# Kernel tuning notes

Hardware: AMD Instinct MI355X
Metric: run time of the kernel (lower is better)

Reference implementation:

```python
import jax, jax.numpy as jnp
import numpy as np

EPS = 1e-08
ORDINAL = 2.0

def setup_inputs() -> dict:
    key = jax.random.key(0)
    k1, k2, k3, k4, k5 = jax.random.split(key, 5)
    B, IN, OUT = 1024, 256, 1024
    inputs = jax.random.normal(k1, (B, IN), dtype=jnp.float32)
    weights = jax.random.normal(k2, (OUT, IN), dtype=jnp.float32) * (1.0 / np.sqrt(IN))
    biases = jax.random.normal(k3, (OUT,), dtype=jnp.float32) * (1.0 / np.sqrt(IN))
    centers = jax.random.normal(k4, (OUT, IN), dtype=jnp.float32) * 0.1
    # diag inv covars ~ U(3/(IN+0.5), 3/(IN-0.5)) per reset_parameters
    inv_covars = jax.random.uniform(k5, (OUT, IN), dtype=jnp.float32,
                                    minval=3.0 / (IN + 0.5), maxval=3.0 / (IN - 0.5))
    return {"inputs": inputs, "weights": weights, "biases": biases,
            "centers": centers, "inv_covars": inv_covars}

def reference(inputs, weights, biases, centers, inv_covars):
    # linear part: [B, OUT]
    l = inputs @ weights.T + biases
    # diag covar path (ordinal = 2.0, so the 1e-32 stabilizer is absent and
    # pow(c^2, 1/ordinal) == |c| after clamping):
    # g[b, z] = sum_i ( |x[b,i] - c[z,i]| * sqrt(clamp(ic[z,i])^2) )^2
    ic = jnp.minimum(inv_covars, 1.0 / EPS)
    scale = jnp.power(ic * ic, 1.0 / ORDINAL)  # [OUT, IN]
    diff = jnp.abs(inputs[:, None, :] - centers[None, :, :]) * scale[None, :, :]  # [B, OUT, IN]
    g = jnp.exp(-jnp.sum(jnp.power(diff, ORDINAL), axis=-1))  # [B, OUT]
    res = l * g
    return (res, g)
```

## Files before the change

### kernel.cpp

```cpp
#include <hip/hip_runtime.h>
#include <hip/hip_bf16.h>
#include <math.h>


typedef __attribute__((ext_vector_type(8))) short short8;
typedef __attribute__((ext_vector_type(4))) float floatx4;

#define MFMA __builtin_amdgcn_mfma_f32_16x16x32_bf16
#define INDIM 256
#define OUTD  1024
#define BD    1024
#define TM 64
#define TN 32
#define TK 64
#define KSTR 72

__device__ __forceinline__ unsigned pkbf(float a, float b) {
    union { __hip_bfloat162 h; unsigned u; } v;
    v.h = __float22bfloat162_rn(make_float2(a, b));
    return v.u;
}

__global__ __launch_bounds__(256)
void fgn_fused(const float* __restrict__ X, const float* __restrict__ W,
               const float* __restrict__ Bias, const float* __restrict__ C,
               const float* __restrict__ IC, float* __restrict__ Out)
{
    __shared__ __align__(16) unsigned short As [TM * KSTR];
    __shared__ __align__(16) unsigned short As2[TM * KSTR];
    __shared__ __align__(16) unsigned short Bw [TN * KSTR];
    __shared__ __align__(16) unsigned short Bg1[TN * KSTR];
    __shared__ __align__(16) unsigned short Bg2[TN * KSTR];
    __shared__ __align__(16) unsigned short Bg3[TN * KSTR];

    const int b    = blockIdx.x;
    const int xcd  = b & 7;
    const int i    = b >> 3;
    const int ncol = xcd + 8 * (i & 3);
    const int mrow = i >> 2;
    const int n0   = ncol * TN;
    const int m0   = mrow * TM;

    const int t    = threadIdx.x;
    const int w    = t >> 6;
    const int lane = t & 63;
    const int r    = lane & 15;
    const int q    = lane >> 4;

    const int arow = t >> 2;
    const int akq  = (t & 3) << 4;
    const int bz   = t >> 3;
    const int bkq  = (t & 7) << 3;

    floatx4 zero = {0.f, 0.f, 0.f, 0.f};
    floatx4 accL[2] = {zero, zero};
    floatx4 accG[2] = {zero, zero};
    floatx4 accC[2] = {zero, zero};
    short8 ones;
    #pragma unroll
    for (int iq = 0; iq < 8; ++iq) ones[iq] = (short)0x3F80;

    for (int k0 = 0; k0 < INDIM; k0 += TK) {
        float4 xa[4];
        {
            const float* xp = &X[(size_t)(m0 + arow) * INDIM + k0 + akq];
            #pragma unroll
            for (int j = 0; j < 4; ++j) xa[j] = ((const float4*)xp)[j];
        }
        const size_t bo = (size_t)(n0 + bz) * INDIM + k0 + bkq;
        float4 wv0 = *(const float4*)&W[bo],  wv1 = *(const float4*)&W[bo + 4];
        float4 cv0 = *(const float4*)&C[bo],  cv1 = *(const float4*)&C[bo + 4];
        float4 iv0 = *(const float4*)&IC[bo], iv1 = *(const float4*)&IC[bo + 4];

        __syncthreads();

        {
            const float* xf = (const float*)xa;
            unsigned ux[8], ux2[8];
            #pragma unroll
            for (int j = 0; j < 8; ++j) {
                float e0 = xf[2*j], e1 = xf[2*j+1];
                ux[j]  = pkbf(e0, e1);
                ux2[j] = pkbf(e0 * e0, e1 * e1);
            }
            uint4* pa  = (uint4*)&As [arow * KSTR + akq];
            uint4* pa2 = (uint4*)&As2[arow * KSTR + akq];
            pa[0]  = make_uint4(ux[0],  ux[1],  ux[2],  ux[3]);
            pa[1]  = make_uint4(ux[4],  ux[5],  ux[6],  ux[7]);
            pa2[0] = make_uint4(ux2[0], ux2[1], ux2[2], ux2[3]);
            pa2[1] = make_uint4(ux2[4], ux2[5], ux2[6], ux2[7]);
        }
        {
            float wf[8] = {wv0.x,wv0.y,wv0.z,wv0.w, wv1.x,wv1.y,wv1.z,wv1.w};
            float cf[8] = {cv0.x,cv0.y,cv0.z,cv0.w, cv1.x,cv1.y,cv1.z,cv1.w};
            float f0[8] = {iv0.x,iv0.y,iv0.z,iv0.w, iv1.x,iv1.y,iv1.z,iv1.w};
            float g1[8], g2[8], g3[8];
            #pragma unroll
            for (int j = 0; j < 8; ++j) {
                float s  = fminf(f0[j], 1e8f);
                float qq = s * s;
                g2[j] = qq;
                g1[j] = -2.f * cf[j] * qq;
                g3[j] = cf[j] * cf[j] * qq;
            }
            const int bb = bz * KSTR + bkq;
            *(uint4*)&Bw [bb] = make_uint4(pkbf(wf[0],wf[1]), pkbf(wf[2],wf[3]),
                                           pkbf(wf[4],wf[5]), pkbf(wf[6],wf[7]));
            *(uint4*)&Bg1[bb] = make_uint4(pkbf(g1[0],g1[1]), pkbf(g1[2],g1[3]),
                                           pkbf(g1[4],g1[5]), pkbf(g1[6],g1[7]));
            *(uint4*)&Bg2[bb] = make_uint4(pkbf(g2[0],g2[1]), pkbf(g2[2],g2[3]),
                                           pkbf(g2[4],g2[5]), pkbf(g2[6],g2[7]));
            *(uint4*)&Bg3[bb] = make_uint4(pkbf(g3[0],g3[1]), pkbf(g3[2],g3[3]),
                                           pkbf(g3[4],g3[5]), pkbf(g3[6],g3[7]));
        }
        __syncthreads();

        #pragma unroll
        for (int kk = 0; kk < 2; ++kk) {
            const int ko = kk * 32 + q * 8;
            short8 a0 = *(const short8*)&As [(w * 16 + r) * KSTR + ko];
            short8 a2 = *(const short8*)&As2[(w * 16 + r) * KSTR + ko];
            #pragma unroll
            for (int nt = 0; nt < 2; ++nt) {
                const int br = (nt * 16 + r) * KSTR + ko;
                short8 bwf = *(const short8*)&Bw [br];
                short8 b1f = *(const short8*)&Bg1[br];
                short8 b2f = *(const short8*)&Bg2[br];
                short8 b3f = *(const short8*)&Bg3[br];
                accL[nt] = MFMA(a0,   bwf, accL[nt], 0, 0, 0);
                accG[nt] = MFMA(a0,   b1f, accG[nt], 0, 0, 0);
                accG[nt] = MFMA(a2,   b2f, accG[nt], 0, 0, 0);
                accC[nt] = MFMA(ones, b3f, accC[nt], 0, 0, 0);
            }
        }
    }

    float* OutR = Out;
    float* OutG = Out + (size_t)BD * OUTD;
    #pragma unroll
    for (int nt = 0; nt < 2; ++nt) {
        const int n     = n0 + nt * 16 + r;
        const float bias = Bias[n];
        const float cz   = accC[nt][0];
        #pragma unroll
        for (int reg = 0; reg < 4; ++reg) {
            const int m = m0 + w * 16 + q * 4 + reg;
            const float g   = expf(-(accG[nt][reg] + cz));
            const float res = (accL[nt][reg] + bias) * g;
            OutR[(size_t)m * OUTD + n] = res;
            OutG[(size_t)m * OUTD + n] = g;
        }
    }
}

extern "C" void kernel_launch(void* const* d_in, const int* in_sizes, int n_in,
                              void* d_out, int out_size, void* d_ws, size_t ws_size,
                              hipStream_t stream) {
    const float* X    = (const float*)d_in[0];
    const float* W    = (const float*)d_in[1];
    const float* Bias = (const float*)d_in[2];
    const float* C    = (const float*)d_in[3];
    const float* IC   = (const float*)d_in[4];
    float* Out = (float*)d_out;

    fgn_fused<<<512, 256, 0, stream>>>(X, W, Bias, C, IC, Out);
}
```

Baseline: 71.55 us.

## Double K-tile size, prefetch next tile, compute center-norm term in fp32

Raises the K tile from 64 to 128, so the kernel runs two iterations, and software-pipelines them by issuing the second tile's global loads before computing on the first. The per-output constant sum c^2*ic^2 is no longer a fourth MFMA against a ones vector. Each thread accumulates it in fp32 and a shuffle reduction writes it to shared memory, which drops one MFMA chain and one LDS buffer. The cost is higher register pressure from the larger prefetch buffers, with launch bounds now requesting two blocks per CU.

```diff
diff --git a/kernel.cpp b/kernel.cpp
--- a/kernel.cpp
+++ b/kernel.cpp
@@ -12,8 +12,8 @@
 #define BD    1024
 #define TM 64
 #define TN 32
-#define TK 64
-#define KSTR 72
+#define TK 128
+#define KSTR 136
 
 __device__ __forceinline__ unsigned pkbf(float a, float b) {
     union { __hip_bfloat162 h; unsigned u; } v;
@@ -21,7 +21,7 @@
     return v.u;
 }
 
-__global__ __launch_bounds__(256)
+__global__ __launch_bounds__(256, 2)
 void fgn_fused(const float* __restrict__ X, const float* __restrict__ W,
                const float* __restrict__ Bias, const float* __restrict__ C,
                const float* __restrict__ IC, float* __restrict__ Out)
@@ -31,15 +31,13 @@
     __shared__ __align__(16) unsigned short Bw [TN * KSTR];
     __shared__ __align__(16) unsigned short Bg1[TN * KSTR];
     __shared__ __align__(16) unsigned short Bg2[TN * KSTR];
-    __shared__ __align__(16) unsigned short Bg3[TN * KSTR];
+    __shared__ float sCz[TN];
 
     const int b    = blockIdx.x;
     const int xcd  = b & 7;
     const int i    = b >> 3;
-    const int ncol = xcd + 8 * (i & 3);
-    const int mrow = i >> 2;
-    const int n0   = ncol * TN;
-    const int m0   = mrow * TM;
+    const int n0   = (xcd + 8 * (i & 3)) * TN;
+    const int m0   = (i >> 2) * TM;
 
     const int t    = threadIdx.x;
     const int w    = t >> 6;
@@ -48,75 +46,73 @@
     const int q    = lane >> 4;
 
     const int arow = t >> 2;
-    const int akq  = (t & 3) << 4;
-    const int bz   = t >> 3;
-    const int bkq  = (t & 7) << 3;
+    const int ak   = (t & 3) << 5;
+    const int brow = t >> 3;
+    const int bk   = (t & 7) << 4;
+
+    float4 xa[8], wv[4], cv[4], iv[4];
+    float czp = 0.f;
+
+    auto loadT = [&](int k0) {
+        const float4* xp = (const float4*)&X[(size_t)(m0 + arow) * INDIM + k0 + ak];
+        #pragma unroll
+        for (int j = 0; j < 8; ++j) xa[j] = xp[j];
+        const size_t bo = (size_t)(n0 + brow) * INDIM + k0 + bk;
+        const float4* wp = (const float4*)&W[bo];
+        const float4* cp = (const float4*)&C[bo];
+        const float4* ip = (const float4*)&IC[bo];
+        #pragma unroll
+        for (int j = 0; j < 4; ++j) { wv[j] = wp[j]; cv[j] = cp[j]; iv[j] = ip[j]; }
+    };
+
+    auto stageT = [&]() {
+        const float* xf = (const float*)xa;
+        uint4* pa  = (uint4*)&As [arow * KSTR + ak];
+        uint4* pa2 = (uint4*)&As2[arow * KSTR + ak];
+        #pragma unroll
+        for (int j = 0; j < 4; ++j) {
+            const float* e = xf + j * 8;
+            pa [j] = make_uint4(pkbf(e[0], e[1]), pkbf(e[2], e[3]),
+                                pkbf(e[4], e[5]), pkbf(e[6], e[7]));
+            pa2[j] = make_uint4(pkbf(e[0]*e[0], e[1]*e[1]), pkbf(e[2]*e[2], e[3]*e[3]),
+                                pkbf(e[4]*e[4], e[5]*e[5]), pkbf(e[6]*e[6], e[7]*e[7]));
+        }
+        const float* wf = (const float*)wv;
+        const float* cf = (const float*)cv;
+        const float* ff = (const float*)iv;
+        const int bb = brow * KSTR + bk;
+        uint4* pw = (uint4*)&Bw [bb];
+        uint4* p1 = (uint4*)&Bg1[bb];
+        uint4* p2 = (uint4*)&Bg2[bb];
+        #pragma unroll
+        for (int j = 0; j < 2; ++j) {
+            float g1[8], g2[8];
+            #pragma unroll
+            for (int e = 0; e < 8; ++e) {
+                const int idx = j * 8 + e;
+                float s  = fminf(ff[idx], 1e8f);
+                float qq = s * s;
+                g2[e] = qq;
+                g1[e] = -2.f * cf[idx] * qq;
+                czp  = fmaf(cf[idx] * cf[idx], qq, czp);
+            }
+            const float* ww = wf + j * 8;
+            pw[j] = make_uint4(pkbf(ww[0], ww[1]), pkbf(ww[2], ww[3]),
+                               pkbf(ww[4], ww[5]), pkbf(ww[6], ww[7]));
+            p1[j] = make_uint4(pkbf(g1[0], g1[1]), pkbf(g1[2], g1[3]),
+                               pkbf(g1[4], g1[5]), pkbf(g1[6], g1[7]));
+            p2[j] = make_uint4(pkbf(g2[0], g2[1]), pkbf(g2[2], g2[3]),
+                               pkbf(g2[4], g2[5]), pkbf(g2[6], g2[7]));
+        }
+    };
 
     floatx4 zero = {0.f, 0.f, 0.f, 0.f};
     floatx4 accL[2] = {zero, zero};
     floatx4 accG[2] = {zero, zero};
-    floatx4 accC[2] = {zero, zero};
-    short8 ones;
-    #pragma unroll
-    for (int iq = 0; iq < 8; ++iq) ones[iq] = (short)0x3F80;
 
-    for (int k0 = 0; k0 < INDIM; k0 += TK) {
-        float4 xa[4];
-        {
-            const float* xp = &X[(size_t)(m0 + arow) * INDIM + k0 + akq];
-            #pragma unroll
-            for (int j = 0; j < 4; ++j) xa[j] = ((const float4*)xp)[j];
-        }
-        const size_t bo = (size_t)(n0 + bz) * INDIM + k0 + bkq;
-        float4 wv0 = *(const float4*)&W[bo],  wv1 = *(const float4*)&W[bo + 4];
-        float4 cv0 = *(const float4*)&C[bo],  cv1 = *(const float4*)&C[bo + 4];
-        float4 iv0 = *(const float4*)&IC[bo], iv1 = *(const float4*)&IC[bo + 4];
-
-        __syncthreads();
-
-        {
-            const float* xf = (const float*)xa;
-            unsigned ux[8], ux2[8];
-            #pragma unroll
-            for (int j = 0; j < 8; ++j) {
-                float e0 = xf[2*j], e1 = xf[2*j+1];
-                ux[j]  = pkbf(e0, e1);
-                ux2[j] = pkbf(e0 * e0, e1 * e1);
-            }
-            uint4* pa  = (uint4*)&As [arow * KSTR + akq];
-            uint4* pa2 = (uint4*)&As2[arow * KSTR + akq];
-            pa[0]  = make_uint4(ux[0],  ux[1],  ux[2],  ux[3]);
-            pa[1]  = make_uint4(ux[4],  ux[5],  ux[6],  ux[7]);
-            pa2[0] = make_uint4(ux2[0], ux2[1], ux2[2], ux2[3]);
-            pa2[1] = make_uint4(ux2[4], ux2[5], ux2[6], ux2[7]);
-        }
-        {
-            float wf[8] = {wv0.x,wv0.y,wv0.z,wv0.w, wv1.x,wv1.y,wv1.z,wv1.w};
-            float cf[8] = {cv0.x,cv0.y,cv0.z,cv0.w, cv1.x,cv1.y,cv1.z,cv1.w};
-            float f0[8] = {iv0.x,iv0.y,iv0.z,iv0.w, iv1.x,iv1.y,iv1.z,iv1.w};
-            float g1[8], g2[8], g3[8];
-            #pragma unroll
-            for (int j = 0; j < 8; ++j) {
-                float s  = fminf(f0[j], 1e8f);
-                float qq = s * s;
-                g2[j] = qq;
-                g1[j] = -2.f * cf[j] * qq;
-                g3[j] = cf[j] * cf[j] * qq;
-            }
-            const int bb = bz * KSTR + bkq;
-            *(uint4*)&Bw [bb] = make_uint4(pkbf(wf[0],wf[1]), pkbf(wf[2],wf[3]),
-                                           pkbf(wf[4],wf[5]), pkbf(wf[6],wf[7]));
-            *(uint4*)&Bg1[bb] = make_uint4(pkbf(g1[0],g1[1]), pkbf(g1[2],g1[3]),
-                                           pkbf(g1[4],g1[5]), pkbf(g1[6],g1[7]));
-            *(uint4*)&Bg2[bb] = make_uint4(pkbf(g2[0],g2[1]), pkbf(g2[2],g2[3]),
-                                           pkbf(g2[4],g2[5]), pkbf(g2[6],g2[7]));
-            *(uint4*)&Bg3[bb] = make_uint4(pkbf(g3[0],g3[1]), pkbf(g3[2],g3[3]),
-                                           pkbf(g3[4],g3[5]), pkbf(g3[6],g3[7]));
-        }
-        __syncthreads();
-
+    auto computeT = [&]() {
         #pragma unroll
-        for (int kk = 0; kk < 2; ++kk) {
+        for (int kk = 0; kk < 4; ++kk) {
             const int ko = kk * 32 + q * 8;
             short8 a0 = *(const short8*)&As [(w * 16 + r) * KSTR + ko];
             short8 a2 = *(const short8*)&As2[(w * 16 + r) * KSTR + ko];
@@ -126,22 +122,34 @@
                 short8 bwf = *(const short8*)&Bw [br];
                 short8 b1f = *(const short8*)&Bg1[br];
                 short8 b2f = *(const short8*)&Bg2[br];
-                short8 b3f = *(const short8*)&Bg3[br];
-                accL[nt] = MFMA(a0,   bwf, accL[nt], 0, 0, 0);
-                accG[nt] = MFMA(a0,   b1f, accG[nt], 0, 0, 0);
-                accG[nt] = MFMA(a2,   b2f, accG[nt], 0, 0, 0);
-                accC[nt] = MFMA(ones, b3f, accC[nt], 0, 0, 0);
+                accL[nt] = MFMA(a0, bwf, accL[nt], 0, 0, 0);
+                accG[nt] = MFMA(a0, b1f, accG[nt], 0, 0, 0);
+                accG[nt] = MFMA(a2, b2f, accG[nt], 0, 0, 0);
             }
         }
-    }
+    };
+
+    loadT(0);
+    stageT();
+    loadT(TK);
+    __syncthreads();
+    computeT();
+    __syncthreads();
+    stageT();
+    czp += __shfl_down(czp, 4);
+    czp += __shfl_down(czp, 2);
+    czp += __shfl_down(czp, 1);
+    if ((t & 7) == 0) sCz[brow] = czp;
+    __syncthreads();
+    computeT();
 
     float* OutR = Out;
     float* OutG = Out + (size_t)BD * OUTD;
     #pragma unroll
     for (int nt = 0; nt < 2; ++nt) {
-        const int n     = n0 + nt * 16 + r;
+        const int n      = n0 + nt * 16 + r;
         const float bias = Bias[n];
-        const float cz   = accC[nt][0];
+        const float cz   = sCz[nt * 16 + r];
         #pragma unroll
         for (int reg = 0; reg < 4; ++reg) {
             const int m = m0 + w * 16 + q * 4 + reg;
```

Result: slower. 72.98 us (+2.0%).

## Halve M tile to double block count; compute center constant in fp32 instead of MFMA

Applied to the files above, without the earlier changes.

Shrinks the row tile from 64 to 32 and launches 1024 blocks, giving each wave one 16x16 output tile instead of two. The per-column constant sum of c^2*ic^2, previously computed by an extra MFMA against a ones vector, is now accumulated in fp32 with a shuffle reduction into shared memory. This removes one MFMA per step and a shared buffer and adds parallelism, but it re-reads W/C/IC transforms twice as often across blocks.

```diff
diff --git a/kernel.cpp b/kernel.cpp
--- a/kernel.cpp
+++ b/kernel.cpp
@@ -10,7 +10,7 @@
 #define INDIM 256
 #define OUTD  1024
 #define BD    1024
-#define TM 64
+#define TM 32
 #define TN 32
 #define TK 64
 #define KSTR 72
@@ -31,125 +31,107 @@
     __shared__ __align__(16) unsigned short Bw [TN * KSTR];
     __shared__ __align__(16) unsigned short Bg1[TN * KSTR];
     __shared__ __align__(16) unsigned short Bg2[TN * KSTR];
-    __shared__ __align__(16) unsigned short Bg3[TN * KSTR];
+    __shared__ float sCz[TN];
 
     const int b    = blockIdx.x;
     const int xcd  = b & 7;
-    const int i    = b >> 3;
-    const int ncol = xcd + 8 * (i & 3);
-    const int mrow = i >> 2;
-    const int n0   = ncol * TN;
-    const int m0   = mrow * TM;
+    const int n0   = (xcd + 8 * ((b >> 3) & 3)) * TN;
+    const int m0   = (b >> 5) * TM;
 
     const int t    = threadIdx.x;
     const int w    = t >> 6;
     const int lane = t & 63;
     const int r    = lane & 15;
     const int q    = lane >> 4;
+    const int mt   = w & 1;
+    const int nt   = w >> 1;
 
-    const int arow = t >> 2;
-    const int akq  = (t & 3) << 4;
-    const int bz   = t >> 3;
-    const int bkq  = (t & 7) << 3;
+    const int srow = t >> 3;
+    const int sk   = (t & 7) << 3;
 
     floatx4 zero = {0.f, 0.f, 0.f, 0.f};
-    floatx4 accL[2] = {zero, zero};
-    floatx4 accG[2] = {zero, zero};
-    floatx4 accC[2] = {zero, zero};
-    short8 ones;
-    #pragma unroll
-    for (int iq = 0; iq < 8; ++iq) ones[iq] = (short)0x3F80;
+    floatx4 accL = zero;
+    floatx4 accG = zero;
+    float czp = 0.f;
 
     for (int k0 = 0; k0 < INDIM; k0 += TK) {
-        float4 xa[4];
-        {
-            const float* xp = &X[(size_t)(m0 + arow) * INDIM + k0 + akq];
-            #pragma unroll
-            for (int j = 0; j < 4; ++j) xa[j] = ((const float4*)xp)[j];
-        }
-        const size_t bo = (size_t)(n0 + bz) * INDIM + k0 + bkq;
-        float4 wv0 = *(const float4*)&W[bo],  wv1 = *(const float4*)&W[bo + 4];
-        float4 cv0 = *(const float4*)&C[bo],  cv1 = *(const float4*)&C[bo + 4];
-        float4 iv0 = *(const float4*)&IC[bo], iv1 = *(const float4*)&IC[bo + 4];
+        const float4* xp = (const float4*)&X[(size_t)(m0 + srow) * INDIM + k0 + sk];
+        float4 x0 = xp[0], x1 = xp[1];
+        const size_t bo = (size_t)(n0 + srow) * INDIM + k0 + sk;
+        const float4* wp = (const float4*)&W[bo];
+        const float4* cp = (const float4*)&C[bo];
+        const float4* ip = (const float4*)&IC[bo];
+        float4 w0 = wp[0], w1 = wp[1];
+        float4 c0 = cp[0], c1 = cp[1];
+        float4 i0 = ip[0], i1 = ip[1];
 
         __syncthreads();
 
         {
-            const float* xf = (const float*)xa;
-            unsigned ux[8], ux2[8];
-            #pragma unroll
-            for (int j = 0; j < 8; ++j) {
-                float e0 = xf[2*j], e1 = xf[2*j+1];
-                ux[j]  = pkbf(e0, e1);
-                ux2[j] = pkbf(e0 * e0, e1 * e1);
-            }
-            uint4* pa  = (uint4*)&As [arow * KSTR + akq];
-            uint4* pa2 = (uint4*)&As2[arow * KSTR + akq];
-            pa[0]  = make_uint4(ux[0],  ux[1],  ux[2],  ux[3]);
-            pa[1]  = make_uint4(ux[4],  ux[5],  ux[6],  ux[7]);
-            pa2[0] = make_uint4(ux2[0], ux2[1], ux2[2], ux2[3]);
-            pa2[1] = make_uint4(ux2[4], ux2[5], ux2[6], ux2[7]);
+            float xf[8] = {x0.x,x0.y,x0.z,x0.w, x1.x,x1.y,x1.z,x1.w};
+            uint4* pa  = (uint4*)&As [srow * KSTR + sk];
+            uint4* pa2 = (uint4*)&As2[srow * KSTR + sk];
+            pa[0]  = make_uint4(pkbf(xf[0],xf[1]), pkbf(xf[2],xf[3]),
+                                pkbf(xf[4],xf[5]), pkbf(xf[6],xf[7]));
+            pa2[0] = make_uint4(pkbf(xf[0]*xf[0],xf[1]*xf[1]), pkbf(xf[2]*xf[2],xf[3]*xf[3]),
+                                pkbf(xf[4]*xf[4],xf[5]*xf[5]), pkbf(xf[6]*xf[6],xf[7]*xf[7]));
         }
         {
-            float wf[8] = {wv0.x,wv0.y,wv0.z,wv0.w, wv1.x,wv1.y,wv1.z,wv1.w};
-            float cf[8] = {cv0.x,cv0.y,cv0.z,cv0.w, cv1.x,cv1.y,cv1.z,cv1.w};
-            float f0[8] = {iv0.x,iv0.y,iv0.z,iv0.w, iv1.x,iv1.y,iv1.z,iv1.w};
-            float g1[8], g2[8], g3[8];
+            float wf[8] = {w0.x,w0.y,w0.z,w0.w, w1.x,w1.y,w1.z,w1.w};
+            float cf[8] = {c0.x,c0.y,c0.z,c0.w, c1.x,c1.y,c1.z,c1.w};
+            float ff[8] = {i0.x,i0.y,i0.z,i0.w, i1.x,i1.y,i1.z,i1.w};
+            float g1[8], g2[8];
             #pragma unroll
-            for (int j = 0; j < 8; ++j) {
-                float s  = fminf(f0[j], 1e8f);
+            for (int e = 0; e < 8; ++e) {
+                float s  = fminf(ff[e], 1e8f);
                 float qq = s * s;
-                g2[j] = qq;
-                g1[j] = -2.f * cf[j] * qq;
-                g3[j] = cf[j] * cf[j] * qq;
+                g2[e] = qq;
+                g1[e] = -2.f * cf[e] * qq;
+                czp  = fmaf(cf[e] * cf[e], qq, czp);
             }
-            const int bb = bz * KSTR + bkq;
+            const int bb = srow * KSTR + sk;
             *(uint4*)&Bw [bb] = make_uint4(pkbf(wf[0],wf[1]), pkbf(wf[2],wf[3]),
                                            pkbf(wf[4],wf[5]), pkbf(wf[6],wf[7]));
             *(uint4*)&Bg1[bb] = make_uint4(pkbf(g1[0],g1[1]), pkbf(g1[2],g1[3]),
                                            pkbf(g1[4],g1[5]), pkbf(g1[6],g1[7]));
             *(uint4*)&Bg2[bb] = make_uint4(pkbf(g2[0],g2[1]), pkbf(g2[2],g2[3]),
                                            pkbf(g2[4],g2[5]), pkbf(g2[6],g2[7]));
-            *(uint4*)&Bg3[bb] = make_uint4(pkbf(g3[0],g3[1]), pkbf(g3[2],g3[3]),
-                                           pkbf(g3[4],g3[5]), pkbf(g3[6],g3[7]));
+        }
+        if (k0 + TK >= INDIM) {
+            czp += __shfl_down(czp, 4);
+            czp += __shfl_down(czp, 2);
+            czp += __shfl_down(czp, 1);
+            if ((t & 7) == 0) sCz[srow] = czp;
         }
         __syncthreads();
 
         #pragma unroll
         for (int kk = 0; kk < 2; ++kk) {
             const int ko = kk * 32 + q * 8;
-            short8 a0 = *(const short8*)&As [(w * 16 + r) * KSTR + ko];
-            short8 a2 = *(const short8*)&As2[(w * 16 + r) * KSTR + ko];
-            #pragma unroll
-            for (int nt = 0; nt < 2; ++nt) {
-                const int br = (nt * 16 + r) * KSTR + ko;
-                short8 bwf = *(const short8*)&Bw [br];
-                short8 b1f = *(const short8*)&Bg1[br];
-                short8 b2f = *(const short8*)&Bg2[br];
-                short8 b3f = *(const short8*)&Bg3[br];
-                accL[nt] = MFMA(a0,   bwf, accL[nt], 0, 0, 0);
-                accG[nt] = MFMA(a0,   b1f, accG[nt], 0, 0, 0);
-                accG[nt] = MFMA(a2,   b2f, accG[nt], 0, 0, 0);
-                accC[nt] = MFMA(ones, b3f, accC[nt], 0, 0, 0);
-            }
+            short8 a0  = *(const short8*)&As [(mt * 16 + r) * KSTR + ko];
+            short8 a2  = *(const short8*)&As2[(mt * 16 + r) * KSTR + ko];
+            const int br = (nt * 16 + r) * KSTR + ko;
+            short8 bwf = *(const short8*)&Bw [br];
+            short8 b1f = *(const short8*)&Bg1[br];
+            short8 b2f = *(const short8*)&Bg2[br];
+            accL = MFMA(a0, bwf, accL, 0, 0, 0);
+            accG = MFMA(a0, b1f, accG, 0, 0, 0);
+            accG = MFMA(a2, b2f, accG, 0, 0, 0);
         }
     }
 
     float* OutR = Out;
     float* OutG = Out + (size_t)BD * OUTD;
+    const int n      = n0 + nt * 16 + r;
+    const float bias = Bias[n];
+    const float cz   = sCz[nt * 16 + r];
     #pragma unroll
-    for (int nt = 0; nt < 2; ++nt) {
-        const int n     = n0 + nt * 16 + r;
-        const float bias = Bias[n];
-        const float cz   = accC[nt][0];
-        #pragma unroll
-        for (int reg = 0; reg < 4; ++reg) {
-            const int m = m0 + w * 16 + q * 4 + reg;
-            const float g   = expf(-(accG[nt][reg] + cz));
-            const float res = (accL[nt][reg] + bias) * g;
-            OutR[(size_t)m * OUTD + n] = res;
-            OutG[(size_t)m * OUTD + n] = g;
-        }
+    for (int reg = 0; reg < 4; ++reg) {
+        const int m = m0 + mt * 16 + q * 4 + reg;
+        const float g   = expf(-(accG[reg] + cz));
+        const float res = (accL[reg] + bias) * g;
+        OutR[(size_t)m * OUTD + n] = res;
+        OutG[(size_t)m * OUTD + n] = g;
     }
 }
 
@@ -163,5 +145,5 @@
     const float* IC   = (const float*)d_in[4];
     float* Out = (float*)d_out;
 
-    fgn_fused<<<512, 256, 0, stream>>>(X, W, Bias, C, IC, Out);
+    fgn_fused<<<1024, 256, 0, stream>>>(X, W, Bias, C, IC, Out);
 }
```

Measured after the change: 70.99 us. Within noise of the previous version (-0.8%).
